# Kernel tuning notes

Hardware: AMD Instinct MI355X
Metric: run time of the kernel (lower is better)

The kernel has to match this reference:

```python
import jax, jax.numpy as jnp
import numpy as np

D_MODEL = 1024
NUM_HEADS = 16
HEAD_DIM = D_MODEL // NUM_HEADS
MAX_SEQ_LEN = 2048
THETA = 10000.0
BATCH = 2
SEQ = 2048


def _rope_tables():
    inv_freq = 1.0 / (THETA ** (jnp.arange(0, HEAD_DIM, 2, dtype=jnp.float32) / HEAD_DIM))
    pos = jnp.arange(MAX_SEQ_LEN, dtype=jnp.float32)
    freqs = pos[:, None] * inv_freq[None, :]  # [max_seq, head_dim/2]
    return jnp.sin(freqs), jnp.cos(freqs)


def _apply_rope(x, sin, cos):
    # x: [b, h, s, d]; sin/cos: [s, d/2] -> broadcast over b, h
    sin = sin[None, None, :, :]
    cos = cos[None, None, :, :]
    x_even = x[..., 0::2]
    x_odd = x[..., 1::2]
    out_even = x_even * cos - x_odd * sin
    out_odd = x_even * sin + x_odd * cos
    # interleave back: stack on new last axis then flatten
    out = jnp.stack((out_even, out_odd), axis=-1)
    return out.reshape(x.shape)


def setup_inputs() -> dict:
    key = jax.random.key(0)
    ks = jax.random.split(key, 5)
    std = (2.0 / (D_MODEL + D_MODEL)) ** 0.5
    return {
        "x": jax.random.normal(ks[0], (BATCH, SEQ, D_MODEL), dtype=jnp.float32),
        "Wq": jax.random.normal(ks[1], (D_MODEL, D_MODEL), dtype=jnp.float32) * std,
        "Wk": jax.random.normal(ks[2], (D_MODEL, D_MODEL), dtype=jnp.float32) * std,
        "Wv": jax.random.normal(ks[3], (D_MODEL, D_MODEL), dtype=jnp.float32) * std,
        "Wo": jax.random.normal(ks[4], (D_MODEL, D_MODEL), dtype=jnp.float32) * std,
    }


def reference(x, Wq, Wk, Wv, Wo):
    b, s, _ = x.shape
    # projections: weight stored [out, in] as in the torch Linear
    Q = jnp.einsum('bsd,od->bso', x, Wq)
    K = jnp.einsum('bsd,od->bso', x, Wk)
    V = jnp.einsum('bsd,od->bso', x, Wv)
    # split heads -> [b, h, s, hd]
    def split(t):
        return t.reshape(b, s, NUM_HEADS, HEAD_DIM).transpose(0, 2, 1, 3)
    Q, K, V = split(Q), split(K), split(V)
    sin, cos = _rope_tables()
    sin, cos = sin[:s], cos[:s]
    Q = _apply_rope(Q, sin, cos)
    K = _apply_rope(K, sin, cos)
    scale = 1.0 / jnp.sqrt(jnp.float32(HEAD_DIM))
    scores = jnp.einsum('bhqd,bhkd->bhqk', Q, K)
    causal = jnp.tril(jnp.ones((s, s), dtype=bool))[None, None]
    scores = jnp.where(causal, scores, -jnp.inf) * scale  # -inf * scale stays -inf
    attn = jax.nn.softmax(scores, axis=-1)
    out = jnp.einsum('bhqk,bhkd->bhqd', attn, V)
    out = out.transpose(0, 2, 1, 3).reshape(b, s, D_MODEL)
    return jnp.einsum('bsd,od->bso', out, Wo)
```

## Files before the change

kernel.cpp:

```cpp
#include <hip/hip_runtime.h>
#include <math.h>

#define NHEADS 16
#define HD 64
#define SEQ 2048
#define BATCH 2
#define DM 1024
#define MTOT (BATCH*SEQ)
#define LDP 72
#define NW 8

typedef __bf16 bf16x8 __attribute__((ext_vector_type(8)));
typedef __bf16 bf16x4 __attribute__((ext_vector_type(4)));
typedef __bf16 bf16x2 __attribute__((ext_vector_type(2)));
typedef float  f32x4  __attribute__((ext_vector_type(4)));

#define LOG2E 1.4426950408889634f

#define GLD16(gp, lp) __builtin_amdgcn_global_load_lds( \
    (const __attribute__((address_space(1))) void*)(gp), \
    (__attribute__((address_space(3))) void*)(lp), 16, 0, 0)

__global__ __launch_bounds__(256)
void cast_all(const float* __restrict__ x, const float* __restrict__ Wq,
              const float* __restrict__ Wk, const float* __restrict__ Wv,
              const float* __restrict__ Wo,
              __bf16* __restrict__ xb, __bf16* __restrict__ Wqkvb,
              __bf16* __restrict__ Wob)
{
    const size_t NX = (size_t)MTOT * DM;
    const size_t NW_ = (size_t)DM * DM;
    const size_t i = ((size_t)blockIdx.x * 256 + threadIdx.x) * 8;
    const float* src; __bf16* dst; size_t off;
    if (i < NX)               { src = x;  dst = xb;            off = i; }
    else if (i < NX + NW_)    { src = Wq; dst = Wqkvb;         off = i - NX; }
    else if (i < NX + 2*NW_)  { src = Wk; dst = Wqkvb + NW_;   off = i - NX - NW_; }
    else if (i < NX + 3*NW_)  { src = Wv; dst = Wqkvb + 2*NW_; off = i - NX - 2*NW_; }
    else                      { src = Wo; dst = Wob;           off = i - NX - 3*NW_; }
    const float4 f0 = *(const float4*)&src[off];
    const float4 f1 = *(const float4*)&src[off + 4];
    bf16x8 o;
    o[0] = (__bf16)f0.x; o[1] = (__bf16)f0.y; o[2] = (__bf16)f0.z; o[3] = (__bf16)f0.w;
    o[4] = (__bf16)f1.x; o[5] = (__bf16)f1.y; o[6] = (__bf16)f1.z; o[7] = (__bf16)f1.w;
    *(bf16x8*)&dst[off] = o;
}

template<int BM, int BN, int MODE>
__global__ __launch_bounds__(256, 3)
void gemm_mfma(const __bf16* __restrict__ A, const __bf16* __restrict__ W,
               float* __restrict__ Cf,
               __bf16* __restrict__ Qb, __bf16* __restrict__ Kb,
               __bf16* __restrict__ Vtb)
{
    constexpr int IT = BM / 32;
    constexpr int JT = BN / 32;
    __shared__ __bf16 As[BM * 64];
    __shared__ __bf16 Bs[BN * 64];

    const int tid  = threadIdx.x;
    const int lane = tid & 63;
    const int wave = tid >> 6;
    const int ll   = lane & 15;
    const int quad = lane >> 4;
    const int wm   = (wave & 1) * (BM / 2);
    const int wn   = (wave >> 1) * (BN / 2);
    const int bm   = blockIdx.x * BM;
    const int bn   = blockIdx.y * BN;

    const __bf16* Ab = A + (size_t)bm * DM;
    const __bf16* Wb = W + (size_t)bn * DM;

    f32x4 acc[IT][JT];
#pragma unroll
    for (int i = 0; i < IT; i++)
#pragma unroll
        for (int j = 0; j < JT; j++) acc[i][j] = (f32x4){0.f, 0.f, 0.f, 0.f};

    for (int k0 = 0; k0 < DM; k0 += 64) {
#pragma unroll
        for (int j = 0; j < BM / 32; j++) {
            const int t = tid + 256 * j;
            const int r = t >> 3, g = t & 7;
            GLD16(Ab + (size_t)r * DM + k0 + ((g ^ (r & 7)) * 8), &As[t * 8]);
        }
#pragma unroll
        for (int j = 0; j < BN / 32; j++) {
            const int t = tid + 256 * j;
            const int r = t >> 3, g = t & 7;
            GLD16(Wb + (size_t)r * DM + k0 + ((g ^ (r & 7)) * 8), &Bs[t * 8]);
        }
        __syncthreads();

#pragma unroll
        for (int kh = 0; kh < 2; kh++) {
            bf16x8 af[IT], bfr[JT];
#pragma unroll
            for (int i = 0; i < IT; i++) {
                const int r = wm + i*16 + ll;
                const int g = kh*4 + quad;
                af[i] = *(const bf16x8*)&As[(r*8 + (g ^ (r & 7))) * 8];
            }
#pragma unroll
            for (int j = 0; j < JT; j++) {
                const int r = wn + j*16 + ll;
                const int g = kh*4 + quad;
                bfr[j] = *(const bf16x8*)&Bs[(r*8 + (g ^ (r & 7))) * 8];
            }
#pragma unroll
            for (int i = 0; i < IT; i++)
#pragma unroll
                for (int j = 0; j < JT; j++)
                    acc[i][j] = __builtin_amdgcn_mfma_f32_16x16x32_bf16(
                        af[i], bfr[j], acc[i][j], 0, 0, 0);
        }
        __syncthreads();
    }

    if (MODE == 1) {
#pragma unroll
        for (int i = 0; i < IT; i++) {
#pragma unroll
            for (int j = 0; j < JT; j++) {
                const int gc = bn + wn + j*16 + ll;
#pragma unroll
                for (int r = 0; r < 4; r++) {
                    const int gr = bm + wm + i*16 + quad*4 + r;
                    Cf[(size_t)gr * DM + gc] = acc[i][j][r];
                }
            }
        }
    } else {
        const int which = bn >> 10;
        const int nb = bn & 1023;
#pragma unroll
        for (int i = 0; i < IT; i++) {
            const int m0 = bm + wm + i*16 + quad*4;
            const int b  = m0 >> 11;
            const int s0 = m0 & (SEQ - 1);
#pragma unroll
            for (int j = 0; j < JT; j++) {
                const int n_g = nb + wn + j*16 + ll;
                const int h = n_g >> 6, d = n_g & (HD - 1);
                if (which == 2) {
                    bf16x4 pk;
#pragma unroll
                    for (int r = 0; r < 4; r++) pk[r] = (__bf16)acc[i][j][r];
                    *(bf16x4*)&Vtb[((size_t)((b*NHEADS + h)*HD + d)) * SEQ + s0] = pk;
                } else {
                    __bf16* P = (which == 0) ? Qb : Kb;
                    const float sc = (which == 0) ? 0.125f * LOG2E : 1.0f;
                    const float inv =
                        exp2f(-(float)(d & ~1) * (13.287712379549449f / 64.0f));
                    const bool odd = (d & 1);
#pragma unroll
                    for (int r = 0; r < 4; r++) {
                        const float own = acc[i][j][r];
                        const float oth = __shfl_xor(own, 1);
                        float sn, cs;
                        __sincosf((float)(s0 + r) * inv, &sn, &cs);
                        const float xe = odd ? oth : own;
                        const float xo = odd ? own : oth;
                        const float o = odd ? (xe * sn + xo * cs)
                                            : (xe * cs - xo * sn);
                        P[((size_t)(b*NHEADS + h) * SEQ + s0 + r) * HD + d] =
                            (__bf16)(o * sc);
                    }
                }
            }
        }
    }
}

__global__ __launch_bounds__(512, 2)
void attn_mfma(const __bf16* __restrict__ Qb, const __bf16* __restrict__ Kb,
               const __bf16* __restrict__ Vtb, __bf16* __restrict__ AOb)
{
    __shared__ __align__(16) __bf16 pt[NW][16][LDP];
    __shared__ float comb[NW][64][17];
    __shared__ float lbuf[NW][64];

    const int tid  = threadIdx.x;
    const int wave = tid >> 6;
    const int lane = tid & 63;
    const int m    = lane & 15;
    const int quad = lane >> 4;
    const int bh   = blockIdx.x;
    const int b    = bh >> 4, h = bh & 15;
    const int qb   = blockIdx.z ? (SEQ/64 - 1) - (int)blockIdx.y : (int)blockIdx.y;
    const int q0   = qb * 64;

    const __bf16* Qp = Qb + (size_t)bh * SEQ * HD;
    const __bf16* Kp = Kb + (size_t)bh * SEQ * HD;
    const __bf16* Vp = Vtb + (size_t)bh * HD * SEQ;

    bf16x8 ones;
#pragma unroll
    for (int j = 0; j < 8; j++) ones[j] = (__bf16)1.0f;

    bf16x8 qf[4][2];
#pragma unroll
    for (int i = 0; i < 4; i++) {
        const __bf16* qp = Qp + (size_t)(q0 + i*16 + m) * HD + quad*8;
        qf[i][0] = *(const bf16x8*)qp;
        qf[i][1] = *(const bf16x8*)(qp + 32);
    }

    f32x4 acc[4][4];
    f32x4 l_acc[4];
#pragma unroll
    for (int i = 0; i < 4; i++) {
        l_acc[i] = (f32x4){0.f, 0.f, 0.f, 0.f};
#pragma unroll
        for (int nt = 0; nt < 4; nt++) acc[i][nt] = (f32x4){0.f, 0.f, 0.f, 0.f};
    }

    for (int t = wave; t <= qb; t += NW) {
        const int k0 = t * 64;
        const bool diag = (t == qb);

        bf16x8 kf[4][2], vf[4][2];
#pragma unroll
        for (int tk = 0; tk < 4; tk++) {
            const __bf16* kp = Kp + (size_t)(k0 + tk*16 + m) * HD + quad*8;
            kf[tk][0] = *(const bf16x8*)kp;
            kf[tk][1] = *(const bf16x8*)(kp + 32);
            const __bf16* vp = Vp + (size_t)(tk*16 + m) * SEQ + k0 + quad*8;
            vf[tk][0] = *(const bf16x8*)vp;
            vf[tk][1] = *(const bf16x8*)(vp + 32);
        }

#pragma unroll
        for (int i = 0; i < 4; i++) {
            f32x4 s[4];
#pragma unroll
            for (int tk = 0; tk < 4; tk++) {
                s[tk] = (f32x4){0.f, 0.f, 0.f, 0.f};
                s[tk] = __builtin_amdgcn_mfma_f32_16x16x32_bf16(
                    qf[i][0], kf[tk][0], s[tk], 0, 0, 0);
                s[tk] = __builtin_amdgcn_mfma_f32_16x16x32_bf16(
                    qf[i][1], kf[tk][1], s[tk], 0, 0, 0);
            }
#pragma unroll
            for (int tk = 0; tk < 4; tk++) {
#pragma unroll
                for (int r = 0; r < 4; r++) {
                    float sv = s[tk][r];
                    if (diag)
                        sv = (16*tk + m <= 16*i + quad*4 + r) ? sv : -INFINITY;
                    const float p = __builtin_amdgcn_exp2f(sv);
                    pt[wave][quad*4 + r][16*tk + m] = (__bf16)p;
                }
            }
            const bf16x8 af0 = *(const bf16x8*)&pt[wave][m][quad*8];
            const bf16x8 af1 = *(const bf16x8*)&pt[wave][m][32 + quad*8];
            l_acc[i] = __builtin_amdgcn_mfma_f32_16x16x32_bf16(
                af0, ones, l_acc[i], 0, 0, 0);
            l_acc[i] = __builtin_amdgcn_mfma_f32_16x16x32_bf16(
                af1, ones, l_acc[i], 0, 0, 0);
#pragma unroll
            for (int nt = 0; nt < 4; nt++) {
                acc[i][nt] = __builtin_amdgcn_mfma_f32_16x16x32_bf16(
                    af0, vf[nt][0], acc[i][nt], 0, 0, 0);
                acc[i][nt] = __builtin_amdgcn_mfma_f32_16x16x32_bf16(
                    af1, vf[nt][1], acc[i][nt], 0, 0, 0);
            }
        }
    }

    if (m == 0) {
#pragma unroll
        for (int i = 0; i < 4; i++)
#pragma unroll
            for (int r = 0; r < 4; r++)
                lbuf[wave][i*16 + quad*4 + r] = l_acc[i][r];
    }
    __syncthreads();

    const int row = tid >> 3;
    const int c0  = (tid & 7) * 2;
    float lsum = 0.f;
#pragma unroll
    for (int w = 0; w < NW; w++) lsum += lbuf[w][row];
    const float rl = 1.0f / lsum;
    __bf16* op = AOb + (size_t)(b * SEQ + q0 + row) * DM + h * HD;

#pragma unroll
    for (int nt = 0; nt < 4; nt++) {
#pragma unroll
        for (int i = 0; i < 4; i++)
#pragma unroll
            for (int r = 0; r < 4; r++)
                comb[wave][i*16 + quad*4 + r][m] = acc[i][nt][r];
        __syncthreads();
        bf16x2 ov;
#pragma unroll
        for (int cc = 0; cc < 2; cc++) {
            const int col = c0 + cc;
            float o = 0.f;
#pragma unroll
            for (int w = 0; w < NW; w++) o += comb[w][row][col];
            ov[cc] = (__bf16)(o * rl);
        }
        *(bf16x2*)&op[nt*16 + c0] = ov;
        if (nt < 3) __syncthreads();
    }
}

extern "C" void kernel_launch(void* const* d_in, const int* in_sizes, int n_in,
                              void* d_out, int out_size, void* d_ws, size_t ws_size,
                              hipStream_t stream) {
    const float* x  = (const float*)d_in[0];
    const float* Wq = (const float*)d_in[1];
    const float* Wk = (const float*)d_in[2];
    const float* Wv = (const float*)d_in[3];
    const float* Wo = (const float*)d_in[4];
    float* out = (float*)d_out;

    char* ws = (char*)d_ws;
    __bf16* xb    = (__bf16*)ws;
    __bf16* Wqkvb = (__bf16*)(ws + ((size_t)8  << 20));
    __bf16* Wob   = (__bf16*)(ws + ((size_t)14 << 20));
    __bf16* Qb    = (__bf16*)(ws + ((size_t)16 << 20));
    __bf16* Kb    = (__bf16*)(ws + ((size_t)24 << 20));
    __bf16* Vtb   = (__bf16*)(ws + ((size_t)32 << 20));
    __bf16* AOb   = (__bf16*)(ws + ((size_t)40 << 20));

    cast_all<<<4096, 256, 0, stream>>>(x, Wq, Wk, Wv, Wo, xb, Wqkvb, Wob);

    gemm_mfma<128,128,0><<<dim3(MTOT/128, 3072/128), 256, 0, stream>>>(
        xb, Wqkvb, nullptr, Qb, Kb, Vtb);

    attn_mfma<<<dim3(BATCH*NHEADS, SEQ/128, 2), 512, 0, stream>>>(
        Qb, Kb, Vtb, AOb);

    gemm_mfma<64,128,1><<<dim3(MTOT/64, DM/128), 256, 0, stream>>>(
        AOb, Wob, out, nullptr, nullptr, nullptr);
}
```

Measured before the change: 181.8 us.

## Rebalance attention into 32-row query blocks with paired causal work per block

The attention kernel moves from 512-thread blocks over 64-row query tiles (8 waves splitting KV tiles) to 256-thread blocks over 32-row query tiles, each block handling a short and a long causal row pair (p and 63-p) in sequence with 4 waves. The intent is to balance causal work across blocks and raise the block count for better occupancy, at the cost of computing the full 64-key diagonal tile for a 32-row query block and running two reduction phases per block. The output projection GEMM also moves from a 64x128 tile to a 128x128 tile, which halves its grid size.

```diff
diff --git a/kernel.cpp b/kernel.cpp
--- a/kernel.cpp
+++ b/kernel.cpp
@@ -8,7 +8,6 @@
 #define DM 1024
 #define MTOT (BATCH*SEQ)
 #define LDP 72
-#define NW 8
 
 typedef __bf16 bf16x8 __attribute__((ext_vector_type(8)));
 typedef __bf16 bf16x4 __attribute__((ext_vector_type(4)));
@@ -171,23 +170,22 @@
     }
 }
 
-__global__ __launch_bounds__(512, 2)
+__global__ __launch_bounds__(256, 2)
 void attn_mfma(const __bf16* __restrict__ Qb, const __bf16* __restrict__ Kb,
                const __bf16* __restrict__ Vtb, __bf16* __restrict__ AOb)
 {
-    __shared__ __align__(16) __bf16 pt[NW][16][LDP];
-    __shared__ float comb[NW][64][17];
-    __shared__ float lbuf[NW][64];
+    __shared__ __align__(16) __bf16 pt[4][16][LDP];
+    __shared__ float comb[4][32][17];
+    __shared__ float lbuf[4][32];
 
     const int tid  = threadIdx.x;
     const int wave = tid >> 6;
     const int lane = tid & 63;
     const int m    = lane & 15;
     const int quad = lane >> 4;
-    const int bh   = blockIdx.x;
+    const int a    = blockIdx.x >> 5;
+    const int bh   = blockIdx.x & 31;
     const int b    = bh >> 4, h = bh & 15;
-    const int qb   = blockIdx.z ? (SEQ/64 - 1) - (int)blockIdx.y : (int)blockIdx.y;
-    const int q0   = qb * 64;
 
     const __bf16* Qp = Qb + (size_t)bh * SEQ * HD;
     const __bf16* Kp = Kb + (size_t)bh * SEQ * HD;
@@ -197,112 +195,116 @@
 #pragma unroll
     for (int j = 0; j < 8; j++) ones[j] = (__bf16)1.0f;
 
-    bf16x8 qf[4][2];
-#pragma unroll
-    for (int i = 0; i < 4; i++) {
-        const __bf16* qp = Qp + (size_t)(q0 + i*16 + m) * HD + quad*8;
-        qf[i][0] = *(const bf16x8*)qp;
-        qf[i][1] = *(const bf16x8*)(qp + 32);
-    }
-
-    f32x4 acc[4][4];
-    f32x4 l_acc[4];
-#pragma unroll
-    for (int i = 0; i < 4; i++) {
-        l_acc[i] = (f32x4){0.f, 0.f, 0.f, 0.f};
-#pragma unroll
-        for (int nt = 0; nt < 4; nt++) acc[i][nt] = (f32x4){0.f, 0.f, 0.f, 0.f};
-    }
-
-    for (int t = wave; t <= qb; t += NW) {
-        const int k0 = t * 64;
-        const bool diag = (t == qb);
-
-        bf16x8 kf[4][2], vf[4][2];
-#pragma unroll
-        for (int tk = 0; tk < 4; tk++) {
-            const __bf16* kp = Kp + (size_t)(k0 + tk*16 + m) * HD + quad*8;
-            kf[tk][0] = *(const bf16x8*)kp;
-            kf[tk][1] = *(const bf16x8*)(kp + 32);
-            const __bf16* vp = Vp + (size_t)(tk*16 + m) * SEQ + k0 + quad*8;
-            vf[tk][0] = *(const bf16x8*)vp;
-            vf[tk][1] = *(const bf16x8*)(vp + 32);
-        }
-
-#pragma unroll
-        for (int i = 0; i < 4; i++) {
-            f32x4 s[4];
+    for (int sel = 0; sel < 2; ++sel) {
+        const int p  = sel ? a : 63 - a;
+        const int q0 = p * 32;
+        const int nk = (p >> 1) + 1;
+
+        bf16x8 qf[2][2];
+#pragma unroll
+        for (int i = 0; i < 2; i++) {
+            const __bf16* qp = Qp + (size_t)(q0 + i*16 + m) * HD + quad*8;
+            qf[i][0] = *(const bf16x8*)qp;
+            qf[i][1] = *(const bf16x8*)(qp + 32);
+        }
+
+        f32x4 acc[2][4];
+        f32x4 l_acc[2];
+#pragma unroll
+        for (int i = 0; i < 2; i++) {
+            l_acc[i] = (f32x4){0.f, 0.f, 0.f, 0.f};
+#pragma unroll
+            for (int nt = 0; nt < 4; nt++) acc[i][nt] = (f32x4){0.f, 0.f, 0.f, 0.f};
+        }
+
+        for (int t = wave; t < nk; t += 4) {
+            const int k0 = t * 64;
+            const bool diag = (t == nk - 1);
+
+            bf16x8 kf[4][2], vf[4][2];
 #pragma unroll
             for (int tk = 0; tk < 4; tk++) {
-                s[tk] = (f32x4){0.f, 0.f, 0.f, 0.f};
-                s[tk] = __builtin_amdgcn_mfma_f32_16x16x32_bf16(
-                    qf[i][0], kf[tk][0], s[tk], 0, 0, 0);
-                s[tk] = __builtin_amdgcn_mfma_f32_16x16x32_bf16(
-                    qf[i][1], kf[tk][1], s[tk], 0, 0, 0);
-            }
-#pragma unroll
-            for (int tk = 0; tk < 4; tk++) {
-#pragma unroll
-                for (int r = 0; r < 4; r++) {
-                    float sv = s[tk][r];
-                    if (diag)
-                        sv = (16*tk + m <= 16*i + quad*4 + r) ? sv : -INFINITY;
-                    const float p = __builtin_amdgcn_exp2f(sv);
-                    pt[wave][quad*4 + r][16*tk + m] = (__bf16)p;
-                }
-            }
-            const bf16x8 af0 = *(const bf16x8*)&pt[wave][m][quad*8];
-            const bf16x8 af1 = *(const bf16x8*)&pt[wave][m][32 + quad*8];
-            l_acc[i] = __builtin_amdgcn_mfma_f32_16x16x32_bf16(
-                af0, ones, l_acc[i], 0, 0, 0);
-            l_acc[i] = __builtin_amdgcn_mfma_f32_16x16x32_bf16(
-                af1, ones, l_acc[i], 0, 0, 0);
-#pragma unroll
-            for (int nt = 0; nt < 4; nt++) {
-                acc[i][nt] = __builtin_amdgcn_mfma_f32_16x16x32_bf16(
-                    af0, vf[nt][0], acc[i][nt], 0, 0, 0);
-                acc[i][nt] = __builtin_amdgcn_mfma_f32_16x16x32_bf16(
-                    af1, vf[nt][1], acc[i][nt], 0, 0, 0);
-            }
-        }
-    }
-
-    if (m == 0) {
-#pragma unroll
-        for (int i = 0; i < 4; i++)
-#pragma unroll
-            for (int r = 0; r < 4; r++)
-                lbuf[wave][i*16 + quad*4 + r] = l_acc[i][r];
-    }
-    __syncthreads();
-
-    const int row = tid >> 3;
-    const int c0  = (tid & 7) * 2;
-    float lsum = 0.f;
-#pragma unroll
-    for (int w = 0; w < NW; w++) lsum += lbuf[w][row];
-    const float rl = 1.0f / lsum;
-    __bf16* op = AOb + (size_t)(b * SEQ + q0 + row) * DM + h * HD;
-
-#pragma unroll
-    for (int nt = 0; nt < 4; nt++) {
-#pragma unroll
-        for (int i = 0; i < 4; i++)
-#pragma unroll
-            for (int r = 0; r < 4; r++)
-                comb[wave][i*16 + quad*4 + r][m] = acc[i][nt][r];
+                const __bf16* kp = Kp + (size_t)(k0 + tk*16 + m) * HD + quad*8;
+                kf[tk][0] = *(const bf16x8*)kp;
+                kf[tk][1] = *(const bf16x8*)(kp + 32);
+                const __bf16* vp = Vp + (size_t)(tk*16 + m) * SEQ + k0 + quad*8;
+                vf[tk][0] = *(const bf16x8*)vp;
+                vf[tk][1] = *(const bf16x8*)(vp + 32);
+            }
+
+#pragma unroll
+            for (int i = 0; i < 2; i++) {
+                f32x4 s[4];
+#pragma unroll
+                for (int tk = 0; tk < 4; tk++) {
+                    s[tk] = (f32x4){0.f, 0.f, 0.f, 0.f};
+                    s[tk] = __builtin_amdgcn_mfma_f32_16x16x32_bf16(
+                        qf[i][0], kf[tk][0], s[tk], 0, 0, 0);
+                    s[tk] = __builtin_amdgcn_mfma_f32_16x16x32_bf16(
+                        qf[i][1], kf[tk][1], s[tk], 0, 0, 0);
+                }
+#pragma unroll
+                for (int tk = 0; tk < 4; tk++) {
+#pragma unroll
+                    for (int r = 0; r < 4; r++) {
+                        float sv = s[tk][r];
+                        if (diag)
+                            sv = (k0 + 16*tk + m <= q0 + 16*i + quad*4 + r)
+                                 ? sv : -INFINITY;
+                        const float pv = __builtin_amdgcn_exp2f(sv);
+                        pt[wave][quad*4 + r][16*tk + m] = (__bf16)pv;
+                    }
+                }
+                const bf16x8 af0 = *(const bf16x8*)&pt[wave][m][quad*8];
+                const bf16x8 af1 = *(const bf16x8*)&pt[wave][m][32 + quad*8];
+                l_acc[i] = __builtin_amdgcn_mfma_f32_16x16x32_bf16(
+                    af0, ones, l_acc[i], 0, 0, 0);
+                l_acc[i] = __builtin_amdgcn_mfma_f32_16x16x32_bf16(
+                    af1, ones, l_acc[i], 0, 0, 0);
+#pragma unroll
+                for (int nt = 0; nt < 4; nt++) {
+                    acc[i][nt] = __builtin_amdgcn_mfma_f32_16x16x32_bf16(
+                        af0, vf[nt][0], acc[i][nt], 0, 0, 0);
+                    acc[i][nt] = __builtin_amdgcn_mfma_f32_16x16x32_bf16(
+                        af1, vf[nt][1], acc[i][nt], 0, 0, 0);
+                }
+            }
+        }
+
+        if (m == 0) {
+#pragma unroll
+            for (int i = 0; i < 2; i++)
+#pragma unroll
+                for (int r = 0; r < 4; r++)
+                    lbuf[wave][i*16 + quad*4 + r] = l_acc[i][r];
+        }
         __syncthreads();
-        bf16x2 ov;
-#pragma unroll
-        for (int cc = 0; cc < 2; cc++) {
-            const int col = c0 + cc;
-            float o = 0.f;
-#pragma unroll
-            for (int w = 0; w < NW; w++) o += comb[w][row][col];
-            ov[cc] = (__bf16)(o * rl);
-        }
-        *(bf16x2*)&op[nt*16 + c0] = ov;
-        if (nt < 3) __syncthreads();
+
+        const int row = tid >> 3;
+        const int c0  = (tid & 7) * 2;
+        const float rl = 1.0f / (lbuf[0][row] + lbuf[1][row]
+                               + lbuf[2][row] + lbuf[3][row]);
+        __bf16* op = AOb + (size_t)(b * SEQ + q0 + row) * DM + h * HD;
+
+#pragma unroll
+        for (int nt = 0; nt < 4; nt++) {
+#pragma unroll
+            for (int i = 0; i < 2; i++)
+#pragma unroll
+                for (int r = 0; r < 4; r++)
+                    comb[wave][i*16 + quad*4 + r][m] = acc[i][nt][r];
+            __syncthreads();
+            bf16x2 ov;
+#pragma unroll
+            for (int cc = 0; cc < 2; cc++) {
+                const int col = c0 + cc;
+                const float o = comb[0][row][col] + comb[1][row][col]
+                              + comb[2][row][col] + comb[3][row][col];
+                ov[cc] = (__bf16)(o * rl);
+            }
+            *(bf16x2*)&op[nt*16 + c0] = ov;
+            __syncthreads();
+        }
     }
 }
 
@@ -330,9 +332,8 @@
     gemm_mfma<128,128,0><<<dim3(MTOT/128, 3072/128), 256, 0, stream>>>(
         xb, Wqkvb, nullptr, Qb, Kb, Vtb);
 
-    attn_mfma<<<dim3(BATCH*NHEADS, SEQ/128, 2), 512, 0, stream>>>(
-        Qb, Kb, Vtb, AOb);
-
-    gemm_mfma<64,128,1><<<dim3(MTOT/64, DM/128), 256, 0, stream>>>(
+    attn_mfma<<<1024, 256, 0, stream>>>(Qb, Kb, Vtb, AOb);
+
+    gemm_mfma<128,128,1><<<dim3(MTOT/128, DM/128), 256, 0, stream>>>(
         AOb, Wob, out, nullptr, nullptr, nullptr);
 }
```

After: 209.3 us. 1.15x slower.
